# Performance work log

Measured on AMD Instinct MI355X. Metric: run time of the kernel, lower is better.

The kernel has to match this reference:

```python
import jax, jax.numpy as jnp
import numpy as np

N_NODES = 100000
N_EDGES = 1600000
NODE_DIM = 128
EDGE_DIM = 32
GLOBAL_DIM = 64
HIDDEN_DIM = 256
N_GRAPHS = 512
IN_DIM = NODE_DIM + EDGE_DIM + GLOBAL_DIM  # 224


def setup_inputs() -> dict:
    key = jax.random.key(0)
    ks = jax.random.split(key, 10)
    x = jax.random.normal(ks[0], (N_NODES, NODE_DIM), dtype=jnp.float32)
    edge_index = jax.random.randint(ks[1], (2, N_EDGES), 0, N_NODES, dtype=jnp.int64)
    edge_attr = jax.random.normal(ks[2], (N_EDGES, EDGE_DIM), dtype=jnp.float32)
    u = jax.random.normal(ks[3], (N_GRAPHS, GLOBAL_DIM), dtype=jnp.float32)
    batch = jnp.sort(jax.random.randint(ks[4], (N_NODES,), 0, N_GRAPHS, dtype=jnp.int64))
    s1 = 1.0 / np.sqrt(IN_DIM)
    s2 = 1.0 / np.sqrt(HIDDEN_DIM)
    W1 = jax.random.uniform(ks[5], (IN_DIM, HIDDEN_DIM), jnp.float32, -s1, s1)
    b1 = jnp.zeros((HIDDEN_DIM,), jnp.float32)
    W2 = jax.random.uniform(ks[6], (HIDDEN_DIM, HIDDEN_DIM), jnp.float32, -s2, s2)
    b2 = jnp.zeros((HIDDEN_DIM,), jnp.float32)
    W3 = jax.random.uniform(ks[7], (HIDDEN_DIM, GLOBAL_DIM), jnp.float32, -s2, s2)
    b3 = jnp.zeros((GLOBAL_DIM,), jnp.float32)
    return {"x": x, "edge_index": edge_index, "edge_attr": edge_attr, "u": u,
            "batch": batch, "W1": W1, "b1": b1, "W2": W2, "b2": b2, "W3": W3, "b3": b3}


def _scatter_mean(vals, seg_ids, num_segments):
    # vals: [M, D], seg_ids: [M] -> [num_segments, D]
    sums = jax.ops.segment_sum(vals, seg_ids, num_segments=num_segments)
    cnt = jax.ops.segment_sum(jnp.ones((vals.shape[0],), vals.dtype), seg_ids,
                              num_segments=num_segments)
    return sums / jnp.maximum(cnt, 1.0)[:, None]


def reference(x, edge_index, edge_attr, u, batch, W1, b1, W2, b2, W3, b3):
    B = u.shape[0]
    node_mean = _scatter_mean(x, batch, B)                      # [B, node_dim]
    edge_seg = batch[edge_index[0]]                             # [E]
    edge_mean = _scatter_mean(edge_attr, edge_seg, B)           # [B, edge_dim]
    out = jnp.concatenate([node_mean, edge_mean, u], axis=1)    # [B, in_dim]
    h = jax.nn.relu(out @ W1 + b1)
    h = jax.nn.relu(h @ W2 + b2)
    return h @ W3 + b3                                          # [B, global_dim]
```

## Files before the change

kernel.cpp:

```cpp
#include <hip/hip_runtime.h>
#include <hip/hip_bf16.h>

#define N_NODES    100000
#define N_EDGES    1600000
#define NODE_DIM   128
#define EDGE_DIM   32
#define GLOBAL_DIM 64
#define HIDDEN_DIM 256
#define N_GRAPHS   512
#define IN_DIM     224
#define ROW33      33

#define EDGE_BLKS  256
#define EDGE_CH    (N_EDGES / EDGE_BLKS)
#define SEG_BLKS   ((N_EDGES / 4 + 255) / 256)
#define BND_BLKS   ((N_NODES + 255) / 256)
#define NSLOT      16
#define SLOTSZ     (N_GRAPHS * ROW33)
#define ZERO_BLKS  ((NSLOT * SLOTSZ / 4 + 255) / 256)
#define GPB        2

#define FXS   1048576.0f
#define FXINV (1.0f / 1048576.0f)

#define WS_NSTART 0
#define WS_NSUM   (WS_NSTART + 1024)
#define WS_ESLOT  (WS_NSUM + N_GRAPHS * NODE_DIM)
#define WS_SEG    (WS_ESLOT + NSLOT * SLOTSZ)

__global__ __launch_bounds__(256) void prep(const int* __restrict__ eidx,
                                            const int* __restrict__ batch,
                                            unsigned short* __restrict__ seg,
                                            int* __restrict__ nstart,
                                            int4* __restrict__ eslot4) {
    const int blk = blockIdx.x;
    if (blk < SEG_BLKS) {
        const int base = (blk * 256 + threadIdx.x) * 4;
        if (base < N_EDGES) {
            const int4 e4 = *reinterpret_cast<const int4*>(eidx + base);
            ushort4 sv;
            sv.x = (unsigned short)batch[e4.x];
            sv.y = (unsigned short)batch[e4.y];
            sv.z = (unsigned short)batch[e4.z];
            sv.w = (unsigned short)batch[e4.w];
            *reinterpret_cast<ushort4*>(seg + base) = sv;
        }
    } else if (blk < SEG_BLKS + BND_BLKS) {
        const int i = (blk - SEG_BLKS) * 256 + threadIdx.x;
        if (i < N_NODES) {
            const int b0 = batch[i];
            if (i == 0)
                for (int g = 0; g <= b0; ++g) nstart[g] = 0;
            if (i < N_NODES - 1) {
                const int b1 = batch[i + 1];
                for (int g = b0 + 1; g <= b1; ++g) nstart[g] = i + 1;
            } else {
                for (int g = b0 + 1; g <= N_GRAPHS; ++g) nstart[g] = N_NODES;
            }
        }
    } else {
        const int i = (blk - SEG_BLKS - BND_BLKS) * 256 + threadIdx.x;
        if (i < NSLOT * SLOTSZ / 4) eslot4[i] = int4{0, 0, 0, 0};
    }
}

__global__ __launch_bounds__(1024) void bulk(const float* __restrict__ eattr,
                                             const unsigned short* __restrict__ seg,
                                             const float* __restrict__ x,
                                             const int* __restrict__ nstart,
                                             int* __restrict__ eslot,
                                             float* __restrict__ nsum) {
    __shared__ int ssum[SLOTSZ];
    const int t = threadIdx.x;

    if (blockIdx.x < EDGE_BLKS) {
        for (int i = t; i < SLOTSZ; i += 1024) ssum[i] = 0;
        __syncthreads();

        const int p = t & 7;
        const int e1 = blockIdx.x * EDGE_CH + EDGE_CH;
#pragma unroll 4
        for (int e = blockIdx.x * EDGE_CH + (t >> 3); e < e1; e += 128) {
            const int s = seg[e];
            const float4 v = *reinterpret_cast<const float4*>(eattr + (size_t)e * EDGE_DIM + p * 4);
            const int b = s * ROW33 + p * 4;
            atomicAdd(&ssum[b + 0], __float2int_rn(v.x * FXS));
            atomicAdd(&ssum[b + 1], __float2int_rn(v.y * FXS));
            atomicAdd(&ssum[b + 2], __float2int_rn(v.z * FXS));
            atomicAdd(&ssum[b + 3], __float2int_rn(v.w * FXS));
            if (p == 0) atomicAdd(&ssum[s * ROW33 + 32], 1);
        }
        __syncthreads();

        int* gs = eslot + (size_t)(blockIdx.x & (NSLOT - 1)) * SLOTSZ;
        for (int i = t; i < SLOTSZ; i += 1024) {
            const int v = ssum[i];
            if (v) atomicAdd(gs + i, v);
        }
    } else {
        const int g = blockIdx.x - EDGE_BLKS;
        const int dp = t & 63;
        const int off = t >> 6;
        const int s0 = nstart[g], e0 = nstart[g + 1];

        float ax0 = 0.f, ay0 = 0.f, ax1 = 0.f, ay1 = 0.f;
        float ax2 = 0.f, ay2 = 0.f, ax3 = 0.f, ay3 = 0.f;
        int r = s0 + off;
        for (; r + 48 < e0; r += 64) {
            const float2 v0 = *reinterpret_cast<const float2*>(x + (size_t)(r     ) * NODE_DIM + dp * 2);
            const float2 v1 = *reinterpret_cast<const float2*>(x + (size_t)(r + 16) * NODE_DIM + dp * 2);
            const float2 v2 = *reinterpret_cast<const float2*>(x + (size_t)(r + 32) * NODE_DIM + dp * 2);
            const float2 v3 = *reinterpret_cast<const float2*>(x + (size_t)(r + 48) * NODE_DIM + dp * 2);
            ax0 += v0.x; ay0 += v0.y; ax1 += v1.x; ay1 += v1.y;
            ax2 += v2.x; ay2 += v2.y; ax3 += v3.x; ay3 += v3.y;
        }
        for (; r < e0; r += 16) {
            const float2 v = *reinterpret_cast<const float2*>(x + (size_t)r * NODE_DIM + dp * 2);
            ax0 += v.x; ay0 += v.y;
        }

        float2* part2 = reinterpret_cast<float2*>(ssum);
        part2[t] = float2{(ax0 + ax1) + (ax2 + ax3), (ay0 + ay1) + (ay2 + ay3)};
        __syncthreads();
        if (t < 64) {
            float sx = 0.f, sy = 0.f;
#pragma unroll 16
            for (int k = 0; k < 16; ++k) {
                const float2 v = part2[t + 64 * k];
                sx += v.x; sy += v.y;
            }
            reinterpret_cast<float2*>(nsum)[(size_t)g * 64 + t] = float2{sx, sy};
        }
    }
}

__global__ __launch_bounds__(256) void finalize_mlp(const float* __restrict__ nsum,
                                                    const int* __restrict__ nstart,
                                                    const int* __restrict__ eslot,
                                                    const float* __restrict__ u,
                                                    const float* __restrict__ W1, const float* __restrict__ b1,
                                                    const float* __restrict__ W2, const float* __restrict__ b2,
                                                    const float* __restrict__ W3, const float* __restrict__ b3,
                                                    float* __restrict__ out) {
    const int g0 = blockIdx.x * GPB;
    const int t = threadIdx.x;
    __shared__ float fs[GPB * IN_DIM];
    __shared__ long long redll[256];
    __shared__ float h[GPB][HIDDEN_DIM];
    __shared__ float h2[GPB][HIDDEN_DIM];
    __shared__ float red[GPB][256];
    __shared__ float s_ecnt[GPB];

    {
        const int col = t & 63, part = t >> 6;
        const int g = col >> 5, d = col & 31;
        long long s = 0;
#pragma unroll 4
        for (int sl = part * 4; sl < part * 4 + 4; ++sl)
            s += eslot[(size_t)sl * SLOTSZ + (size_t)(g0 + g) * ROW33 + d];
        redll[t] = s;
    }
    if (t < GPB) {
        int c = 0;
#pragma unroll 16
        for (int sl = 0; sl < NSLOT; ++sl)
            c += eslot[(size_t)sl * SLOTSZ + (size_t)(g0 + t) * ROW33 + 32];
        s_ecnt[t] = fmaxf((float)c, 1.f);
    }
    __syncthreads();

    {
        const int g = t >> 7, d = t & 127;
        const float cnt = fmaxf((float)(nstart[g0 + g + 1] - nstart[g0 + g]), 1.f);
        fs[g * IN_DIM + d] = nsum[(size_t)(g0 + g) * NODE_DIM + d] / cnt;
    }
    if (t < 64) {
        const long long tot = redll[t] + redll[t + 64] + redll[t + 128] + redll[t + 192];
        const int g = t >> 5, d = t & 31;
        fs[g * IN_DIM + NODE_DIM + d] = ((float)tot * FXINV) / s_ecnt[g];
    } else if (t < 192) {
        const int i = t - 64, g = i >> 6, c = i & 63;
        fs[g * IN_DIM + NODE_DIM + EDGE_DIM + c] = u[(size_t)(g0 + g) * GLOBAL_DIM + c];
    }
    __syncthreads();

    float acc0, acc1;
    const float bb1 = b1[t];
    acc0 = acc1 = bb1;
    for (int k = 0; k < IN_DIM; ++k) {
        const float w = W1[k * HIDDEN_DIM + t];
        acc0 = fmaf(fs[k], w, acc0);
        acc1 = fmaf(fs[IN_DIM + k], w, acc1);
    }
    h[0][t] = fmaxf(acc0, 0.f); h[1][t] = fmaxf(acc1, 0.f);
    __syncthreads();

    const float bb2 = b2[t];
    acc0 = acc1 = bb2;
    for (int k = 0; k < HIDDEN_DIM; ++k) {
        const float w = W2[k * HIDDEN_DIM + t];
        acc0 = fmaf(h[0][k], w, acc0);
        acc1 = fmaf(h[1][k], w, acc1);
    }
    h2[0][t] = fmaxf(acc0, 0.f); h2[1][t] = fmaxf(acc1, 0.f);
    __syncthreads();

    const int c3 = t & 63, q = t >> 6;
    acc0 = acc1 = 0.f;
    for (int k = q * 64; k < q * 64 + 64; ++k) {
        const float w = W3[k * GLOBAL_DIM + c3];
        acc0 = fmaf(h2[0][k], w, acc0);
        acc1 = fmaf(h2[1][k], w, acc1);
    }
    red[0][t] = acc0; red[1][t] = acc1;
    __syncthreads();
    if (t < GPB * GLOBAL_DIM) {
        const int g = t >> 6, c = t & 63;
        out[(size_t)(g0 + g) * GLOBAL_DIM + c] = red[g][c] + red[g][c + 64] +
                                                 red[g][c + 128] + red[g][c + 192] + b3[c];
    }
}

extern "C" void kernel_launch(void* const* d_in, const int* in_sizes, int n_in,
                              void* d_out, int out_size, void* d_ws, size_t ws_size,
                              hipStream_t stream) {
    const float* x         = (const float*)d_in[0];
    const int*   edge_idx  = (const int*)d_in[1];
    const float* edge_attr = (const float*)d_in[2];
    const float* u         = (const float*)d_in[3];
    const int*   batch     = (const int*)d_in[4];
    const float* W1 = (const float*)d_in[5];
    const float* b1 = (const float*)d_in[6];
    const float* W2 = (const float*)d_in[7];
    const float* b2 = (const float*)d_in[8];
    const float* W3 = (const float*)d_in[9];
    const float* b3 = (const float*)d_in[10];
    float* out = (float*)d_out;

    int* ws32 = (int*)d_ws;
    int*            nstart = ws32 + WS_NSTART;
    float*          nsum   = (float*)(ws32 + WS_NSUM);
    int*            eslot  = ws32 + WS_ESLOT;
    unsigned short* seg    = (unsigned short*)(ws32 + WS_SEG);

    prep<<<SEG_BLKS + BND_BLKS + ZERO_BLKS, 256, 0, stream>>>(edge_idx, batch, seg, nstart,
                                                              (int4*)eslot);
    bulk<<<EDGE_BLKS + N_GRAPHS, 1024, 0, stream>>>(edge_attr, seg, x, nstart, eslot, nsum);
    finalize_mlp<<<N_GRAPHS / GPB, 256, 0, stream>>>(nsum, nstart, eslot, u,
                                                     W1, b1, W2, b2, W3, b3, out);
}
```

Before: 90.56 us.

## Fuse prep, reduction and MLP into one cooperative kernel with grid syncs

```diff
diff --git a/kernel.cpp b/kernel.cpp
--- a/kernel.cpp
+++ b/kernel.cpp
@@ -1,5 +1,7 @@
 #include <hip/hip_runtime.h>
 #include <hip/hip_bf16.h>
+#include <hip/hip_cooperative_groups.h>
+namespace cg = cooperative_groups;
 
 #define N_NODES    100000
 #define N_EDGES    1600000
@@ -11,14 +13,12 @@
 #define IN_DIM     224
 #define ROW33      33
 
-#define EDGE_BLKS  256
-#define EDGE_CH    (N_EDGES / EDGE_BLKS)
-#define SEG_BLKS   ((N_EDGES / 4 + 255) / 256)
-#define BND_BLKS   ((N_NODES + 255) / 256)
+#define NBLK       256
+#define NTHR       1024
+#define TOTTHR     (NBLK * NTHR)
+#define EDGE_CH    (N_EDGES / NBLK)
 #define NSLOT      16
 #define SLOTSZ     (N_GRAPHS * ROW33)
-#define ZERO_BLKS  ((NSLOT * SLOTSZ / 4 + 255) / 256)
-#define GPB        2
 
 #define FXS   1048576.0f
 #define FXINV (1.0f / 1048576.0f)
@@ -28,59 +28,57 @@
 #define WS_ESLOT  (WS_NSUM + N_GRAPHS * NODE_DIM)
 #define WS_SEG    (WS_ESLOT + NSLOT * SLOTSZ)
 
-__global__ __launch_bounds__(256) void prep(const int* __restrict__ eidx,
-                                            const int* __restrict__ batch,
-                                            unsigned short* __restrict__ seg,
-                                            int* __restrict__ nstart,
-                                            int4* __restrict__ eslot4) {
+__global__ __launch_bounds__(NTHR) void fused(
+    const float* __restrict__ x, const int* __restrict__ eidx,
+    const float* __restrict__ eattr, const float* __restrict__ u,
+    const int* __restrict__ batch,
+    const float* __restrict__ W1, const float* __restrict__ b1,
+    const float* __restrict__ W2, const float* __restrict__ b2,
+    const float* __restrict__ W3, const float* __restrict__ b3,
+    float* __restrict__ out,
+    int* __restrict__ nstart, float* __restrict__ nsum,
+    int* __restrict__ eslot, unsigned short* __restrict__ seg)
+{
+    __shared__ int ssum[SLOTSZ];
+    cg::grid_group grid = cg::this_grid();
+    const int t = threadIdx.x;
     const int blk = blockIdx.x;
-    if (blk < SEG_BLKS) {
-        const int base = (blk * 256 + threadIdx.x) * 4;
-        if (base < N_EDGES) {
-            const int4 e4 = *reinterpret_cast<const int4*>(eidx + base);
-            ushort4 sv;
-            sv.x = (unsigned short)batch[e4.x];
-            sv.y = (unsigned short)batch[e4.y];
-            sv.z = (unsigned short)batch[e4.z];
-            sv.w = (unsigned short)batch[e4.w];
-            *reinterpret_cast<ushort4*>(seg + base) = sv;
-        }
-    } else if (blk < SEG_BLKS + BND_BLKS) {
-        const int i = (blk - SEG_BLKS) * 256 + threadIdx.x;
-        if (i < N_NODES) {
-            const int b0 = batch[i];
-            if (i == 0)
-                for (int g = 0; g <= b0; ++g) nstart[g] = 0;
-            if (i < N_NODES - 1) {
-                const int b1 = batch[i + 1];
-                for (int g = b0 + 1; g <= b1; ++g) nstart[g] = i + 1;
-            } else {
-                for (int g = b0 + 1; g <= N_GRAPHS; ++g) nstart[g] = N_NODES;
-            }
-        }
-    } else {
-        const int i = (blk - SEG_BLKS - BND_BLKS) * 256 + threadIdx.x;
-        if (i < NSLOT * SLOTSZ / 4) eslot4[i] = int4{0, 0, 0, 0};
-    }
-}
-
-__global__ __launch_bounds__(1024) void bulk(const float* __restrict__ eattr,
-                                             const unsigned short* __restrict__ seg,
-                                             const float* __restrict__ x,
-                                             const int* __restrict__ nstart,
-                                             int* __restrict__ eslot,
-                                             float* __restrict__ nsum) {
-    __shared__ int ssum[SLOTSZ];
-    const int t = threadIdx.x;
-
-    if (blockIdx.x < EDGE_BLKS) {
-        for (int i = t; i < SLOTSZ; i += 1024) ssum[i] = 0;
-        __syncthreads();
-
+    const int gtid = blk * NTHR + t;
+
+    for (int i = gtid; i < N_EDGES / 4; i += TOTTHR) {
+        const int4 e4 = reinterpret_cast<const int4*>(eidx)[i];
+        ushort4 sv;
+        sv.x = (unsigned short)batch[e4.x];
+        sv.y = (unsigned short)batch[e4.y];
+        sv.z = (unsigned short)batch[e4.z];
+        sv.w = (unsigned short)batch[e4.w];
+        reinterpret_cast<ushort4*>(seg)[i] = sv;
+    }
+    if (gtid < N_NODES) {
+        const int b0 = batch[gtid];
+        if (gtid == 0)
+            for (int g = 0; g <= b0; ++g) nstart[g] = 0;
+        if (gtid < N_NODES - 1) {
+            const int b1v = batch[gtid + 1];
+            for (int g = b0 + 1; g <= b1v; ++g) nstart[g] = gtid + 1;
+        } else {
+            for (int g = b0 + 1; g <= N_GRAPHS; ++g) nstart[g] = N_NODES;
+        }
+    }
+    if (gtid < NSLOT * SLOTSZ / 4)
+        reinterpret_cast<int4*>(eslot)[gtid] = int4{0, 0, 0, 0};
+
+    __threadfence();
+    grid.sync();
+
+    for (int i = t; i < SLOTSZ; i += NTHR) ssum[i] = 0;
+    __syncthreads();
+
+    {
         const int p = t & 7;
-        const int e1 = blockIdx.x * EDGE_CH + EDGE_CH;
+        const int e1 = blk * EDGE_CH + EDGE_CH;
 #pragma unroll 4
-        for (int e = blockIdx.x * EDGE_CH + (t >> 3); e < e1; e += 128) {
+        for (int e = blk * EDGE_CH + (t >> 3); e < e1; e += 128) {
             const int s = seg[e];
             const float4 v = *reinterpret_cast<const float4*>(eattr + (size_t)e * EDGE_DIM + p * 4);
             const int b = s * ROW33 + p * 4;
@@ -90,15 +88,19 @@
             atomicAdd(&ssum[b + 3], __float2int_rn(v.w * FXS));
             if (p == 0) atomicAdd(&ssum[s * ROW33 + 32], 1);
         }
-        __syncthreads();
-
-        int* gs = eslot + (size_t)(blockIdx.x & (NSLOT - 1)) * SLOTSZ;
-        for (int i = t; i < SLOTSZ; i += 1024) {
+    }
+    __syncthreads();
+    {
+        int* gs = eslot + (size_t)(blk & (NSLOT - 1)) * SLOTSZ;
+        for (int i = t; i < SLOTSZ; i += NTHR) {
             const int v = ssum[i];
             if (v) atomicAdd(gs + i, v);
         }
-    } else {
-        const int g = blockIdx.x - EDGE_BLKS;
+    }
+    __syncthreads();
+
+    for (int gi = 0; gi < 2; ++gi) {
+        const int g = blk * 2 + gi;
         const int dp = t & 63;
         const int off = t >> 6;
         const int s0 = nstart[g], e0 = nstart[g + 1];
@@ -120,6 +122,7 @@
         }
 
         float2* part2 = reinterpret_cast<float2*>(ssum);
+        __syncthreads();
         part2[t] = float2{(ax0 + ax1) + (ax2 + ax3), (ay0 + ay1) + (ay2 + ay3)};
         __syncthreads();
         if (t < 64) {
@@ -132,92 +135,65 @@
             reinterpret_cast<float2*>(nsum)[(size_t)g * 64 + t] = float2{sx, sy};
         }
     }
-}
-
-__global__ __launch_bounds__(256) void finalize_mlp(const float* __restrict__ nsum,
-                                                    const int* __restrict__ nstart,
-                                                    const int* __restrict__ eslot,
-                                                    const float* __restrict__ u,
-                                                    const float* __restrict__ W1, const float* __restrict__ b1,
-                                                    const float* __restrict__ W2, const float* __restrict__ b2,
-                                                    const float* __restrict__ W3, const float* __restrict__ b3,
-                                                    float* __restrict__ out) {
-    const int g0 = blockIdx.x * GPB;
-    const int t = threadIdx.x;
-    __shared__ float fs[GPB * IN_DIM];
-    __shared__ long long redll[256];
-    __shared__ float h[GPB][HIDDEN_DIM];
-    __shared__ float h2[GPB][HIDDEN_DIM];
-    __shared__ float red[GPB][256];
-    __shared__ float s_ecnt[GPB];
-
+
+    __threadfence();
+    grid.sync();
+
+    if (blk >= N_GRAPHS / 4) return;
     {
-        const int col = t & 63, part = t >> 6;
-        const int g = col >> 5, d = col & 31;
-        long long s = 0;
-#pragma unroll 4
-        for (int sl = part * 4; sl < part * 4 + 4; ++sl)
-            s += eslot[(size_t)sl * SLOTSZ + (size_t)(g0 + g) * ROW33 + d];
-        redll[t] = s;
-    }
-    if (t < GPB) {
-        int c = 0;
+        const int gl = t >> 8;
+        const int c  = t & 255;
+        const int g  = blk * 4 + gl;
+
+        int*   sE = ssum;
+        float* fs = reinterpret_cast<float*>(&ssum[144]);
+        float* hh = fs + 4 * IN_DIM;
+        float* h2 = hh + 4 * HIDDEN_DIM;
+        float* rd = h2 + 4 * HIDDEN_DIM;
+
+        if (c < 33) {
+            int s = 0;
 #pragma unroll 16
-        for (int sl = 0; sl < NSLOT; ++sl)
-            c += eslot[(size_t)sl * SLOTSZ + (size_t)(g0 + t) * ROW33 + 32];
-        s_ecnt[t] = fmaxf((float)c, 1.f);
-    }
-    __syncthreads();
-
-    {
-        const int g = t >> 7, d = t & 127;
-        const float cnt = fmaxf((float)(nstart[g0 + g + 1] - nstart[g0 + g]), 1.f);
-        fs[g * IN_DIM + d] = nsum[(size_t)(g0 + g) * NODE_DIM + d] / cnt;
-    }
-    if (t < 64) {
-        const long long tot = redll[t] + redll[t + 64] + redll[t + 128] + redll[t + 192];
-        const int g = t >> 5, d = t & 31;
-        fs[g * IN_DIM + NODE_DIM + d] = ((float)tot * FXINV) / s_ecnt[g];
-    } else if (t < 192) {
-        const int i = t - 64, g = i >> 6, c = i & 63;
-        fs[g * IN_DIM + NODE_DIM + EDGE_DIM + c] = u[(size_t)(g0 + g) * GLOBAL_DIM + c];
-    }
-    __syncthreads();
-
-    float acc0, acc1;
-    const float bb1 = b1[t];
-    acc0 = acc1 = bb1;
-    for (int k = 0; k < IN_DIM; ++k) {
-        const float w = W1[k * HIDDEN_DIM + t];
-        acc0 = fmaf(fs[k], w, acc0);
-        acc1 = fmaf(fs[IN_DIM + k], w, acc1);
-    }
-    h[0][t] = fmaxf(acc0, 0.f); h[1][t] = fmaxf(acc1, 0.f);
-    __syncthreads();
-
-    const float bb2 = b2[t];
-    acc0 = acc1 = bb2;
-    for (int k = 0; k < HIDDEN_DIM; ++k) {
-        const float w = W2[k * HIDDEN_DIM + t];
-        acc0 = fmaf(h[0][k], w, acc0);
-        acc1 = fmaf(h[1][k], w, acc1);
-    }
-    h2[0][t] = fmaxf(acc0, 0.f); h2[1][t] = fmaxf(acc1, 0.f);
-    __syncthreads();
-
-    const int c3 = t & 63, q = t >> 6;
-    acc0 = acc1 = 0.f;
-    for (int k = q * 64; k < q * 64 + 64; ++k) {
-        const float w = W3[k * GLOBAL_DIM + c3];
-        acc0 = fmaf(h2[0][k], w, acc0);
-        acc1 = fmaf(h2[1][k], w, acc1);
-    }
-    red[0][t] = acc0; red[1][t] = acc1;
-    __syncthreads();
-    if (t < GPB * GLOBAL_DIM) {
-        const int g = t >> 6, c = t & 63;
-        out[(size_t)(g0 + g) * GLOBAL_DIM + c] = red[g][c] + red[g][c + 64] +
-                                                 red[g][c + 128] + red[g][c + 192] + b3[c];
+            for (int sl = 0; sl < NSLOT; ++sl)
+                s += eslot[(size_t)sl * SLOTSZ + (size_t)g * ROW33 + c];
+            sE[gl * 33 + c] = s;
+        }
+        __syncthreads();
+
+        if (c < NODE_DIM) {
+            const float cnt = fmaxf((float)(nstart[g + 1] - nstart[g]), 1.f);
+            fs[gl * IN_DIM + c] = nsum[(size_t)g * NODE_DIM + c] / cnt;
+        } else if (c < NODE_DIM + EDGE_DIM) {
+            const int d = c - NODE_DIM;
+            const float ec = fmaxf((float)sE[gl * 33 + 32], 1.f);
+            fs[gl * IN_DIM + c] = ((float)sE[gl * 33 + d] * FXINV) / ec;
+        } else if (c < IN_DIM) {
+            fs[gl * IN_DIM + c] = u[(size_t)g * GLOBAL_DIM + (c - NODE_DIM - EDGE_DIM)];
+        }
+        __syncthreads();
+
+        float acc = b1[c];
+        const float* fsg = fs + gl * IN_DIM;
+        for (int k = 0; k < IN_DIM; ++k) acc = fmaf(fsg[k], W1[k * HIDDEN_DIM + c], acc);
+        hh[gl * HIDDEN_DIM + c] = fmaxf(acc, 0.f);
+        __syncthreads();
+
+        acc = b2[c];
+        const float* hg = hh + gl * HIDDEN_DIM;
+        for (int k = 0; k < HIDDEN_DIM; ++k) acc = fmaf(hg[k], W2[k * HIDDEN_DIM + c], acc);
+        h2[gl * HIDDEN_DIM + c] = fmaxf(acc, 0.f);
+        __syncthreads();
+
+        const int col = c & 63, q = c >> 6;
+        acc = 0.f;
+        const float* h2g = h2 + gl * HIDDEN_DIM;
+        for (int k = q * 64; k < q * 64 + 64; ++k) acc = fmaf(h2g[k], W3[k * GLOBAL_DIM + col], acc);
+        rd[gl * 256 + c] = acc;
+        __syncthreads();
+        if (c < GLOBAL_DIM) {
+            out[(size_t)g * GLOBAL_DIM + c] = rd[gl * 256 + c] + rd[gl * 256 + c + 64] +
+                                              rd[gl * 256 + c + 128] + rd[gl * 256 + c + 192] + b3[c];
+        }
     }
 }
 
@@ -243,9 +219,11 @@
     int*            eslot  = ws32 + WS_ESLOT;
     unsigned short* seg    = (unsigned short*)(ws32 + WS_SEG);
 
-    prep<<<SEG_BLKS + BND_BLKS + ZERO_BLKS, 256, 0, stream>>>(edge_idx, batch, seg, nstart,
-                                                              (int4*)eslot);
-    bulk<<<EDGE_BLKS + N_GRAPHS, 1024, 0, stream>>>(edge_attr, seg, x, nstart, eslot, nsum);
-    finalize_mlp<<<N_GRAPHS / GPB, 256, 0, stream>>>(nsum, nstart, eslot, u,
-                                                     W1, b1, W2, b2, W3, b3, out);
+    void* args[] = {
+        (void*)&x, (void*)&edge_idx, (void*)&edge_attr, (void*)&u, (void*)&batch,
+        (void*)&W1, (void*)&b1, (void*)&W2, (void*)&b2, (void*)&W3, (void*)&b3,
+        (void*)&out, (void*)&nstart, (void*)&nsum, (void*)&eslot, (void*)&seg
+    };
+    hipLaunchCooperativeKernel((const void*)fused, dim3(NBLK), dim3(NTHR),
+                               args, 0, stream);
 }
```

New measurement: 330.2 us. 3.65x slower.

## Drop prep kernel: inline segment lookup, binary-search node ranges, per-block edge slots

Applied to the files above, without the earlier changes.

```diff
diff --git a/kernel.cpp b/kernel.cpp
--- a/kernel.cpp
+++ b/kernel.cpp
@@ -13,63 +13,23 @@
 
 #define EDGE_BLKS  256
 #define EDGE_CH    (N_EDGES / EDGE_BLKS)
-#define SEG_BLKS   ((N_EDGES / 4 + 255) / 256)
-#define BND_BLKS   ((N_NODES + 255) / 256)
-#define NSLOT      16
 #define SLOTSZ     (N_GRAPHS * ROW33)
-#define ZERO_BLKS  ((NSLOT * SLOTSZ / 4 + 255) / 256)
 #define GPB        2
 
 #define FXS   1048576.0f
 #define FXINV (1.0f / 1048576.0f)
 
-#define WS_NSTART 0
-#define WS_NSUM   (WS_NSTART + 1024)
-#define WS_ESLOT  (WS_NSUM + N_GRAPHS * NODE_DIM)
-#define WS_SEG    (WS_ESLOT + NSLOT * SLOTSZ)
-
-__global__ __launch_bounds__(256) void prep(const int* __restrict__ eidx,
-                                            const int* __restrict__ batch,
-                                            unsigned short* __restrict__ seg,
-                                            int* __restrict__ nstart,
-                                            int4* __restrict__ eslot4) {
-    const int blk = blockIdx.x;
-    if (blk < SEG_BLKS) {
-        const int base = (blk * 256 + threadIdx.x) * 4;
-        if (base < N_EDGES) {
-            const int4 e4 = *reinterpret_cast<const int4*>(eidx + base);
-            ushort4 sv;
-            sv.x = (unsigned short)batch[e4.x];
-            sv.y = (unsigned short)batch[e4.y];
-            sv.z = (unsigned short)batch[e4.z];
-            sv.w = (unsigned short)batch[e4.w];
-            *reinterpret_cast<ushort4*>(seg + base) = sv;
-        }
-    } else if (blk < SEG_BLKS + BND_BLKS) {
-        const int i = (blk - SEG_BLKS) * 256 + threadIdx.x;
-        if (i < N_NODES) {
-            const int b0 = batch[i];
-            if (i == 0)
-                for (int g = 0; g <= b0; ++g) nstart[g] = 0;
-            if (i < N_NODES - 1) {
-                const int b1 = batch[i + 1];
-                for (int g = b0 + 1; g <= b1; ++g) nstart[g] = i + 1;
-            } else {
-                for (int g = b0 + 1; g <= N_GRAPHS; ++g) nstart[g] = N_NODES;
-            }
-        }
-    } else {
-        const int i = (blk - SEG_BLKS - BND_BLKS) * 256 + threadIdx.x;
-        if (i < NSLOT * SLOTSZ / 4) eslot4[i] = int4{0, 0, 0, 0};
-    }
-}
+#define WS_NSUM   0
+#define WS_NCNT   (WS_NSUM + N_GRAPHS * NODE_DIM)
+#define WS_ESLOT  (WS_NCNT + N_GRAPHS)
 
 __global__ __launch_bounds__(1024) void bulk(const float* __restrict__ eattr,
-                                             const unsigned short* __restrict__ seg,
+                                             const int* __restrict__ eidx,
                                              const float* __restrict__ x,
-                                             const int* __restrict__ nstart,
+                                             const int* __restrict__ batch,
                                              int* __restrict__ eslot,
-                                             float* __restrict__ nsum) {
+                                             float* __restrict__ nsum,
+                                             float* __restrict__ ncnt) {
     __shared__ int ssum[SLOTSZ];
     const int t = threadIdx.x;
 
@@ -77,12 +37,23 @@
         for (int i = t; i < SLOTSZ; i += 1024) ssum[i] = 0;
         __syncthreads();
 
+        const float4* eattr4 = reinterpret_cast<const float4*>(eattr);
         const int p = t & 7;
         const int e1 = blockIdx.x * EDGE_CH + EDGE_CH;
-#pragma unroll 4
-        for (int e = blockIdx.x * EDGE_CH + (t >> 3); e < e1; e += 128) {
-            const int s = seg[e];
-            const float4 v = *reinterpret_cast<const float4*>(eattr + (size_t)e * EDGE_DIM + p * 4);
+        int e = blockIdx.x * EDGE_CH + (t >> 3);
+
+        int    s_nxt = (e < e1) ? batch[eidx[e]] : 0;
+        float4 v_nxt = (e < e1) ? eattr4[(size_t)e * 8 + p] : float4{0.f, 0.f, 0.f, 0.f};
+
+#pragma unroll 2
+        for (; e < e1; e += 128) {
+            const int s = s_nxt;
+            const float4 v = v_nxt;
+            const int en = e + 128;
+            if (en < e1) {
+                s_nxt = batch[eidx[en]];
+                v_nxt = eattr4[(size_t)en * 8 + p];
+            }
             const int b = s * ROW33 + p * 4;
             atomicAdd(&ssum[b + 0], __float2int_rn(v.x * FXS));
             atomicAdd(&ssum[b + 1], __float2int_rn(v.y * FXS));
@@ -92,17 +63,25 @@
         }
         __syncthreads();
 
-        int* gs = eslot + (size_t)(blockIdx.x & (NSLOT - 1)) * SLOTSZ;
-        for (int i = t; i < SLOTSZ; i += 1024) {
-            const int v = ssum[i];
-            if (v) atomicAdd(gs + i, v);
-        }
+        int* gs = eslot + (size_t)blockIdx.x * SLOTSZ;
+        for (int i = t; i < SLOTSZ; i += 1024) gs[i] = ssum[i];
     } else {
         const int g = blockIdx.x - EDGE_BLKS;
+        __shared__ int sb[2];
+        if (t < 2) {
+            const int target = g + t;
+            int lo = 0, hi = N_NODES;
+            while (lo < hi) {
+                const int mid = (lo + hi) >> 1;
+                if (batch[mid] < target) lo = mid + 1; else hi = mid;
+            }
+            sb[t] = lo;
+        }
+        __syncthreads();
+        const int s0 = sb[0], e0 = sb[1];
+
         const int dp = t & 63;
         const int off = t >> 6;
-        const int s0 = nstart[g], e0 = nstart[g + 1];
-
         float ax0 = 0.f, ay0 = 0.f, ax1 = 0.f, ay1 = 0.f;
         float ax2 = 0.f, ay2 = 0.f, ax3 = 0.f, ay3 = 0.f;
         int r = s0 + off;
@@ -131,11 +110,12 @@
             }
             reinterpret_cast<float2*>(nsum)[(size_t)g * 64 + t] = float2{sx, sy};
         }
+        if (t == 0) ncnt[g] = fmaxf((float)(e0 - s0), 1.f);
     }
 }
 
 __global__ __launch_bounds__(256) void finalize_mlp(const float* __restrict__ nsum,
-                                                    const int* __restrict__ nstart,
+                                                    const float* __restrict__ ncnt,
                                                     const int* __restrict__ eslot,
                                                     const float* __restrict__ u,
                                                     const float* __restrict__ W1, const float* __restrict__ b1,
@@ -146,6 +126,7 @@
     const int t = threadIdx.x;
     __shared__ float fs[GPB * IN_DIM];
     __shared__ long long redll[256];
+    __shared__ long long redcnt[8];
     __shared__ float h[GPB][HIDDEN_DIM];
     __shared__ float h2[GPB][HIDDEN_DIM];
     __shared__ float red[GPB][256];
@@ -155,25 +136,28 @@
         const int col = t & 63, part = t >> 6;
         const int g = col >> 5, d = col & 31;
         long long s = 0;
-#pragma unroll 4
-        for (int sl = part * 4; sl < part * 4 + 4; ++sl)
+#pragma unroll 8
+        for (int sl = part * 64; sl < part * 64 + 64; ++sl)
             s += eslot[(size_t)sl * SLOTSZ + (size_t)(g0 + g) * ROW33 + d];
         redll[t] = s;
     }
-    if (t < GPB) {
-        int c = 0;
-#pragma unroll 16
-        for (int sl = 0; sl < NSLOT; ++sl)
-            c += eslot[(size_t)sl * SLOTSZ + (size_t)(g0 + t) * ROW33 + 32];
-        s_ecnt[t] = fmaxf((float)c, 1.f);
-    }
-    __syncthreads();
+    if (t < 8) {
+        const int g = t & 1, part = t >> 1;
+        long long c = 0;
+#pragma unroll 8
+        for (int sl = part * 64; sl < part * 64 + 64; ++sl)
+            c += eslot[(size_t)sl * SLOTSZ + (size_t)(g0 + g) * ROW33 + 32];
+        redcnt[t] = c;
+    }
+    __syncthreads();
+    if (t < GPB)
+        s_ecnt[t] = fmaxf((float)(redcnt[t] + redcnt[t + 2] + redcnt[t + 4] + redcnt[t + 6]), 1.f);
 
     {
         const int g = t >> 7, d = t & 127;
-        const float cnt = fmaxf((float)(nstart[g0 + g + 1] - nstart[g0 + g]), 1.f);
-        fs[g * IN_DIM + d] = nsum[(size_t)(g0 + g) * NODE_DIM + d] / cnt;
-    }
+        fs[g * IN_DIM + d] = nsum[(size_t)(g0 + g) * NODE_DIM + d] / ncnt[g0 + g];
+    }
+    __syncthreads();
     if (t < 64) {
         const long long tot = redll[t] + redll[t + 64] + redll[t + 128] + redll[t + 192];
         const int g = t >> 5, d = t & 31;
@@ -238,14 +222,12 @@
     float* out = (float*)d_out;
 
     int* ws32 = (int*)d_ws;
-    int*            nstart = ws32 + WS_NSTART;
-    float*          nsum   = (float*)(ws32 + WS_NSUM);
-    int*            eslot  = ws32 + WS_ESLOT;
-    unsigned short* seg    = (unsigned short*)(ws32 + WS_SEG);
-
-    prep<<<SEG_BLKS + BND_BLKS + ZERO_BLKS, 256, 0, stream>>>(edge_idx, batch, seg, nstart,
-                                                              (int4*)eslot);
-    bulk<<<EDGE_BLKS + N_GRAPHS, 1024, 0, stream>>>(edge_attr, seg, x, nstart, eslot, nsum);
-    finalize_mlp<<<N_GRAPHS / GPB, 256, 0, stream>>>(nsum, nstart, eslot, u,
+    float* nsum  = (float*)(ws32 + WS_NSUM);
+    float* ncnt  = (float*)(ws32 + WS_NCNT);
+    int*   eslot = ws32 + WS_ESLOT;
+
+    bulk<<<EDGE_BLKS + N_GRAPHS, 1024, 0, stream>>>(edge_attr, edge_idx, x, batch,
+                                                    eslot, nsum, ncnt);
+    finalize_mlp<<<N_GRAPHS / GPB, 256, 0, stream>>>(nsum, ncnt, eslot, u,
                                                      W1, b1, W2, b2, W3, b3, out);
 }
```

New measurement: 90.92 us. About the same (+0.4%).
